# Optimization experiments

Measured on AMD Instinct MI355X. Metric: run time of the kernel, lower is better.

Reference implementation:

```python
import jax, jax.numpy as jnp
import numpy as np

N, D, F, C = 50000, 32, 128, 16
LN_EPS = 1e-5
CLAMP_MIN = 1e-5


def _layernorm_1d(x):
    # LayerNorm over the full node vector, no affine (elementwise_affine=False)
    m = x.mean()
    v = x.var()  # biased, matches torch LayerNorm
    return (x - m) / jnp.sqrt(v + LN_EPS)


def setup_inputs() -> dict:
    key = jax.random.key(0)
    k1, k2, k3, k4, k5, k6 = jax.random.split(key, 6)
    return {
        "h": jax.random.normal(k1, (N, F), dtype=jnp.float32),
        "logits": jax.random.normal(k2, (N, C), dtype=jnp.float32),
        "old_z": jax.random.uniform(k3, (N,), dtype=jnp.float32),
        "tau_1": jax.random.uniform(k4, (1,), dtype=jnp.float32),
        "tau_2": jax.random.uniform(k5, (1,), dtype=jnp.float32),
        "nbr": jax.random.randint(k6, (N, D), 0, N, dtype=jnp.int32),
    }


def reference(h, logits, old_z, tau_1, tau_2, nbr):
    # --- mailbox pass 1: neighbor logits -> adaptive gating features ---
    pred = jnp.argmax(logits[nbr], axis=2)          # [N, D] neighbor class preds
    center_pred = jnp.argmax(logits, axis=1)        # [N]
    # n_degree = 1 in the source (counts, not fractions) -- reproduced faithfully
    f1 = jnp.sum(pred == center_pred[:, None], axis=1).astype(h.dtype)  # [N]
    cnts = jax.nn.one_hot(pred, C, dtype=h.dtype).sum(axis=1)           # [N, C]
    cnts_p = jnp.clip(cnts, CLAMP_MIN, None)
    f2 = -jnp.sum(cnts_p * jnp.log(cnts_p), axis=1)                     # [N]
    f1 = jax.lax.stop_gradient(f1)
    f2 = jax.lax.stop_gradient(f2)

    norm_f1 = _layernorm_1d(f1)
    norm_f2 = _layernorm_1d(f2)
    # shared_tau=True path: tau_1, tau_2 passed in ([1] broadcasts over [N])
    z = jax.nn.sigmoid(-(norm_f1 - tau_1)) * jax.nn.sigmoid(-(norm_f2 - tau_2))  # [N]
    gate = jnp.minimum(old_z, z)

    # --- mailbox pass 2: scatter-sum of neighbor features ---
    agg = h[nbr].sum(axis=1)                        # [N, F]
    normagg = jax.nn.relu(agg)
    new_h = h + gate[:, None] * normagg
    return new_h, z
```

## Files before the change

### kernel.cpp

```cpp
#include <hip/hip_runtime.h>
#include <math.h>

#define NN 50000
#define DEG 32
#define FDIM 128
#define NCLS 16
#define LN_EPS 1e-5f
#define CLAMP_MIN 1e-5f

#define PRED_NB 196
#define CONV_NB 512
#define NGROUPS (NN * FDIM / 8)
#define FEAT_NB ((NN * 8 + 255) / 256)

typedef float  nf4 __attribute__((ext_vector_type(4)));
typedef unsigned nu4 __attribute__((ext_vector_type(4)));

__device__ inline unsigned bf_rne(float x) {
    unsigned u = __float_as_uint(x);
    u += 0x7fffu + ((u >> 16) & 1u);
    return u >> 16;
}

__global__ __launch_bounds__(256) void k_pre(const float* __restrict__ logits,
                                             unsigned char* __restrict__ pred8,
                                             const float* __restrict__ h,
                                             unsigned* __restrict__ hb) {
    int b = blockIdx.x;
    if (b < PRED_NB) {
        int i = b * 256 + threadIdx.x;
        if (i >= NN) return;
        const nf4* lp = (const nf4*)(logits + (long)i * NCLS);
        float best = -INFINITY;
        int bi = 0;
#pragma unroll
        for (int q = 0; q < 4; ++q) {
            nf4 v = __builtin_nontemporal_load(lp + q);
#pragma unroll
            for (int r = 0; r < 4; ++r) {
                if (v[r] > best) { best = v[r]; bi = q * 4 + r; }
            }
        }
        pred8[i] = (unsigned char)bi;
    } else {
        int g0 = (b - PRED_NB) * 256 + threadIdx.x;
        for (int g = g0; g < NGROUPS; g += CONV_NB * 256) {
            const nf4* src = (const nf4*)(h + (long)g * 8);
            nf4 a = __builtin_nontemporal_load(src);
            nf4 c = __builtin_nontemporal_load(src + 1);
            nu4 o;
            o.x = bf_rne(a.x) | (bf_rne(a.y) << 16);
            o.y = bf_rne(a.z) | (bf_rne(a.w) << 16);
            o.z = bf_rne(c.x) | (bf_rne(c.y) << 16);
            o.w = bf_rne(c.z) | (bf_rne(c.w) << 16);
            ((nu4*)hb)[g] = o;
        }
    }
}

__global__ __launch_bounds__(256) void k_feats8(const int* __restrict__ nbr,
                                                const unsigned char* __restrict__ pred8,
                                                float* __restrict__ f1,
                                                float* __restrict__ f2,
                                                float* __restrict__ partials, int n) {
    int g = blockIdx.x * 256 + threadIdx.x;
    int node = g >> 3;
    int sub = g & 7;
    bool valid = (node < n);
    unsigned long long lo = 0ull, hi = 0ull;
    if (valid) {
        int4 k4 = ((const int4*)(nbr + (long)node * DEG))[sub];
        int ks[4] = {k4.x, k4.y, k4.z, k4.w};
#pragma unroll
        for (int r = 0; r < 4; ++r) {
            int p = pred8[ks[r]];
            unsigned long long inc = 1ull << ((p & 7) * 8);
            if (p < 8) lo += inc; else hi += inc;
        }
    }
#pragma unroll
    for (int m = 1; m <= 4; m <<= 1) {
        lo += __shfl_xor(lo, m);
        hi += __shfl_xor(hi, m);
    }
    float v1 = 0.f, v2 = 0.f;
    if (valid && sub == 0) {
        int cp = pred8[node];
        unsigned long long src = (cp < 8) ? lo : hi;
        v1 = (float)((src >> ((cp & 7) * 8)) & 0xffull);
        float ent = 0.f;
#pragma unroll
        for (int c = 0; c < NCLS; ++c) {
            unsigned long long s = (c < 8) ? lo : hi;
            float cnt = (float)((s >> ((c & 7) * 8)) & 0xffull);
            float x = fmaxf(cnt, CLAMP_MIN);
            ent -= x * logf(x);
        }
        v2 = ent;
        f1[node] = v1;
        f2[node] = v2;
    }
    float s0 = v1, s1 = v1 * v1, s2 = v2, s3 = v2 * v2;
#pragma unroll
    for (int off = 8; off <= 32; off <<= 1) {
        s0 += __shfl_down(s0, off);
        s1 += __shfl_down(s1, off);
        s2 += __shfl_down(s2, off);
        s3 += __shfl_down(s3, off);
    }
    __shared__ float red[4][4];
    int wid = threadIdx.x >> 6;
    if ((threadIdx.x & 63) == 0) {
        red[wid][0] = s0; red[wid][1] = s1; red[wid][2] = s2; red[wid][3] = s3;
    }
    __syncthreads();
    if (threadIdx.x == 0) {
        float t0 = 0.f, t1 = 0.f, t2 = 0.f, t3 = 0.f;
#pragma unroll
        for (int w = 0; w < 4; ++w) {
            t0 += red[w][0]; t1 += red[w][1]; t2 += red[w][2]; t3 += red[w][3];
        }
        float* pp = partials + (long)blockIdx.x * 4;
        pp[0] = t0; pp[1] = t1; pp[2] = t2; pp[3] = t3;
    }
}

__global__ __launch_bounds__(256) void k_params(const float* __restrict__ partials,
                                                int nb, float* __restrict__ params) {
    double s0 = 0, s1 = 0, s2 = 0, s3 = 0;
    for (int b = threadIdx.x; b < nb; b += 256) {
        const float* pp = partials + (long)b * 4;
        s0 += (double)pp[0]; s1 += (double)pp[1];
        s2 += (double)pp[2]; s3 += (double)pp[3];
    }
#pragma unroll
    for (int off = 32; off > 0; off >>= 1) {
        s0 += __shfl_down(s0, off);
        s1 += __shfl_down(s1, off);
        s2 += __shfl_down(s2, off);
        s3 += __shfl_down(s3, off);
    }
    __shared__ double red[4][4];
    int wid = threadIdx.x >> 6;
    if ((threadIdx.x & 63) == 0) {
        red[wid][0] = s0; red[wid][1] = s1; red[wid][2] = s2; red[wid][3] = s3;
    }
    __syncthreads();
    if (threadIdx.x == 0) {
        double t0 = 0, t1 = 0, t2 = 0, t3 = 0;
        for (int w = 0; w < 4; ++w) {
            t0 += red[w][0]; t1 += red[w][1]; t2 += red[w][2]; t3 += red[w][3];
        }
        double inv_n = 1.0 / (double)NN;
        double m1 = t0 * inv_n;
        double var1 = t1 * inv_n - m1 * m1;
        double m2 = t2 * inv_n;
        double var2 = t3 * inv_n - m2 * m2;
        params[0] = (float)m1;
        params[1] = (float)(1.0 / sqrt(var1 + (double)LN_EPS));
        params[2] = (float)m2;
        params[3] = (float)(1.0 / sqrt(var2 + (double)LN_EPS));
    }
}

__global__ __launch_bounds__(256) void k_agg_bf(const unsigned* __restrict__ hb,
                                                const int* __restrict__ nbr,
                                                const float* __restrict__ old_z,
                                                const float* __restrict__ tau1,
                                                const float* __restrict__ tau2,
                                                const float* __restrict__ f1,
                                                const float* __restrict__ f2,
                                                const float* __restrict__ params,
                                                float* __restrict__ out_h,
                                                float* __restrict__ out_z, int n) {
    int t = blockIdx.x * 256 + threadIdx.x;
    int node = t >> 5;
    int lane = threadIdx.x & 31;
    if (node >= n) return;
    int k = __builtin_nontemporal_load(nbr + (long)node * DEG + lane);
    float4 acc = make_float4(0.f, 0.f, 0.f, 0.f);
#pragma unroll
    for (int jj = 0; jj < 4; ++jj) {
        uint2 vs[8];
#pragma unroll
        for (int j = 0; j < 8; ++j) {
            int kj = __shfl(k, jj * 8 + j, 32);
            vs[j] = ((const uint2*)(hb + (long)kj * (FDIM / 2)))[lane];
        }
#pragma unroll
        for (int j = 0; j < 8; ++j) {
            acc.x += __uint_as_float(vs[j].x << 16);
            acc.y += __uint_as_float(vs[j].x & 0xffff0000u);
            acc.z += __uint_as_float(vs[j].y << 16);
            acc.w += __uint_as_float(vs[j].y & 0xffff0000u);
        }
    }
    float a = (f1[node] - params[0]) * params[1] - tau1[0];
    float b = (f2[node] - params[2]) * params[3] - tau2[0];
    float z = 1.f / ((1.f + expf(a)) * (1.f + expf(b)));
    float gate = fminf(old_z[node], z);
    uint2 hid = ((const uint2*)(hb + (long)node * (FDIM / 2)))[lane];
    nf4 o;
    o.x = __uint_as_float(hid.x << 16)        + gate * fmaxf(acc.x, 0.f);
    o.y = __uint_as_float(hid.x & 0xffff0000u) + gate * fmaxf(acc.y, 0.f);
    o.z = __uint_as_float(hid.y << 16)        + gate * fmaxf(acc.z, 0.f);
    o.w = __uint_as_float(hid.y & 0xffff0000u) + gate * fmaxf(acc.w, 0.f);
    __builtin_nontemporal_store(o, (nf4*)(out_h + (long)node * FDIM) + lane);
    if (lane == 0) __builtin_nontemporal_store(z, out_z + node);
}

extern "C" void kernel_launch(void* const* d_in, const int* in_sizes, int n_in,
                              void* d_out, int out_size, void* d_ws, size_t ws_size,
                              hipStream_t stream) {
    const float* h      = (const float*)d_in[0];
    const float* logits = (const float*)d_in[1];
    const float* old_z  = (const float*)d_in[2];
    const float* tau1   = (const float*)d_in[3];
    const float* tau2   = (const float*)d_in[4];
    const int*   nbr    = (const int*)d_in[5];

    char* ws = (char*)d_ws;
    float*         params   = (float*)ws;
    float*         partials = (float*)(ws + 64);
    unsigned char* pred8    = (unsigned char*)(ws + 32768);
    float*         f1       = (float*)(ws + 90112);
    float*         f2       = (float*)(ws + 294912);
    unsigned*      hb       = (unsigned*)(ws + 524288);

    float* out_h = (float*)d_out;
    float* out_z = out_h + (long)NN * FDIM;

    k_pre   <<<PRED_NB + CONV_NB, 256, 0, stream>>>(logits, pred8, h, hb);
    k_feats8<<<FEAT_NB, 256, 0, stream>>>(nbr, pred8, f1, f2, partials, NN);
    k_params<<<1, 256, 0, stream>>>(partials, FEAT_NB, params);
    k_agg_bf<<<(NN * DEG + 255) / 256, 256, 0, stream>>>(hb, nbr, old_z, tau1, tau2,
                                                         f1, f2, params, out_h, out_z, NN);
}
```

Before: 148.7 us.

## Stage class predictions in LDS and compute features one node per thread

The gating-feature kernel now copies the full 50 KB prediction byte array into shared memory in each block. Each thread then handles one whole node, looking up all 32 neighbour predictions in LDS instead of issuing global byte gathers, which removes the cross-lane shuffle combine. The trade-off is that every one of the 196 blocks re-reads 50 KB from global memory, and the large LDS footprint limits occupancy to roughly one block per CU. The per-thread neighbour-list reads are also no longer coalesced across lanes.

```diff
diff --git a/kernel.cpp b/kernel.cpp
--- a/kernel.cpp
+++ b/kernel.cpp
@@ -11,7 +11,7 @@
 #define PRED_NB 196
 #define CONV_NB 512
 #define NGROUPS (NN * FDIM / 8)
-#define FEAT_NB ((NN * 8 + 255) / 256)
+#define FEAT_NB 196
 
 typedef float  nf4 __attribute__((ext_vector_type(4)));
 typedef unsigned nu4 __attribute__((ext_vector_type(4)));
@@ -58,34 +58,35 @@
     }
 }
 
-__global__ __launch_bounds__(256) void k_feats8(const int* __restrict__ nbr,
-                                                const unsigned char* __restrict__ pred8,
-                                                float* __restrict__ f1,
-                                                float* __restrict__ f2,
-                                                float* __restrict__ partials, int n) {
-    int g = blockIdx.x * 256 + threadIdx.x;
-    int node = g >> 3;
-    int sub = g & 7;
-    bool valid = (node < n);
-    unsigned long long lo = 0ull, hi = 0ull;
-    if (valid) {
-        int4 k4 = ((const int4*)(nbr + (long)node * DEG))[sub];
-        int ks[4] = {k4.x, k4.y, k4.z, k4.w};
-#pragma unroll
-        for (int r = 0; r < 4; ++r) {
-            int p = pred8[ks[r]];
-            unsigned long long inc = 1ull << ((p & 7) * 8);
-            if (p < 8) lo += inc; else hi += inc;
-        }
-    }
-#pragma unroll
-    for (int m = 1; m <= 4; m <<= 1) {
-        lo += __shfl_xor(lo, m);
-        hi += __shfl_xor(hi, m);
-    }
+__global__ __launch_bounds__(256) void k_feats_lds(const int* __restrict__ nbr,
+                                                   const unsigned char* __restrict__ pred8,
+                                                   float* __restrict__ f1,
+                                                   float* __restrict__ f2,
+                                                   float* __restrict__ partials, int n) {
+    __shared__ unsigned char lp[NN];
+    {
+        const uint4* s4 = (const uint4*)pred8;
+        uint4* d4 = (uint4*)lp;
+        for (int i = threadIdx.x; i < 3125; i += 256) d4[i] = s4[i];
+    }
+    __syncthreads();
+    int node = blockIdx.x * 256 + threadIdx.x;
     float v1 = 0.f, v2 = 0.f;
-    if (valid && sub == 0) {
-        int cp = pred8[node];
+    if (node < n) {
+        unsigned long long lo = 0ull, hi = 0ull;
+        const int4* np = (const int4*)(nbr + (long)node * DEG);
+#pragma unroll
+        for (int q = 0; q < 8; ++q) {
+            int4 k4 = np[q];
+            int ks[4] = {k4.x, k4.y, k4.z, k4.w};
+#pragma unroll
+            for (int r = 0; r < 4; ++r) {
+                int p = lp[ks[r]];
+                unsigned long long inc = 1ull << ((p & 7) * 8);
+                if (p < 8) lo += inc; else hi += inc;
+            }
+        }
+        int cp = lp[node];
         unsigned long long src = (cp < 8) ? lo : hi;
         v1 = (float)((src >> ((cp & 7) * 8)) & 0xffull);
         float ent = 0.f;
@@ -102,7 +103,7 @@
     }
     float s0 = v1, s1 = v1 * v1, s2 = v2, s3 = v2 * v2;
 #pragma unroll
-    for (int off = 8; off <= 32; off <<= 1) {
+    for (int off = 32; off > 0; off >>= 1) {
         s0 += __shfl_down(s0, off);
         s1 += __shfl_down(s1, off);
         s2 += __shfl_down(s2, off);
@@ -201,9 +202,9 @@
     float gate = fminf(old_z[node], z);
     uint2 hid = ((const uint2*)(hb + (long)node * (FDIM / 2)))[lane];
     nf4 o;
-    o.x = __uint_as_float(hid.x << 16)        + gate * fmaxf(acc.x, 0.f);
+    o.x = __uint_as_float(hid.x << 16)         + gate * fmaxf(acc.x, 0.f);
     o.y = __uint_as_float(hid.x & 0xffff0000u) + gate * fmaxf(acc.y, 0.f);
-    o.z = __uint_as_float(hid.y << 16)        + gate * fmaxf(acc.z, 0.f);
+    o.z = __uint_as_float(hid.y << 16)         + gate * fmaxf(acc.z, 0.f);
     o.w = __uint_as_float(hid.y & 0xffff0000u) + gate * fmaxf(acc.w, 0.f);
     __builtin_nontemporal_store(o, (nf4*)(out_h + (long)node * FDIM) + lane);
     if (lane == 0) __builtin_nontemporal_store(z, out_z + node);
@@ -230,9 +231,9 @@
     float* out_h = (float*)d_out;
     float* out_z = out_h + (long)NN * FDIM;
 
-    k_pre   <<<PRED_NB + CONV_NB, 256, 0, stream>>>(logits, pred8, h, hb);
-    k_feats8<<<FEAT_NB, 256, 0, stream>>>(nbr, pred8, f1, f2, partials, NN);
-    k_params<<<1, 256, 0, stream>>>(partials, FEAT_NB, params);
-    k_agg_bf<<<(NN * DEG + 255) / 256, 256, 0, stream>>>(hb, nbr, old_z, tau1, tau2,
-                                                         f1, f2, params, out_h, out_z, NN);
-}
+    k_pre     <<<PRED_NB + CONV_NB, 256, 0, stream>>>(logits, pred8, h, hb);
+    k_feats_lds<<<FEAT_NB, 256, 0, stream>>>(nbr, pred8, f1, f2, partials, NN);
+    k_params  <<<1, 256, 0, stream>>>(partials, FEAT_NB, params);
+    k_agg_bf  <<<(NN * DEG + 255) / 256, 256, 0, stream>>>(hb, nbr, old_z, tau1, tau2,
+                                                           f1, f2, params, out_h, out_z, NN);
+}
```

Result: no change. 147.5 us (-0.8%).
